# Kernel tuning notes

Measured on AMD Instinct MI355X. Metric: run time of the kernel, lower is better.

The kernel has to match this reference:

```python
import jax, jax.numpy as jnp
import numpy as np

DIM = 512
NUM_HEADS = 8
HEAD_DIM = DIM // NUM_HEADS
FFN_MULT = 4
B, N = 4, 2048
EPS = 1e-5


def setup_inputs() -> dict:
    key = jax.random.key(0)
    ks = jax.random.split(key, 12)
    s = 0.02
    return {
        "H": jax.random.normal(ks[0], (B, N, DIM), jnp.float32),
        "A": jax.random.uniform(ks[1], (B, N, N), jnp.float32),
        "ln1_g": jnp.ones((DIM,), jnp.float32),
        "ln1_b": jnp.zeros((DIM,), jnp.float32),
        "qkv_w": jax.random.normal(ks[2], (DIM, 3 * DIM), jnp.float32) * s,
        "qkv_b": jnp.zeros((3 * DIM,), jnp.float32),
        "proj_w": jax.random.normal(ks[3], (DIM, DIM), jnp.float32) * s,
        "proj_b": jnp.zeros((DIM,), jnp.float32),
        "ln2_g": jnp.ones((DIM,), jnp.float32),
        "ln2_b": jnp.zeros((DIM,), jnp.float32),
        "w1": jax.random.normal(ks[4], (DIM, DIM * FFN_MULT), jnp.float32) * s,
        "b1": jnp.zeros((DIM * FFN_MULT,), jnp.float32),
        "w2": jax.random.normal(ks[5], (DIM * FFN_MULT, DIM), jnp.float32) * s,
        "b2": jnp.zeros((DIM,), jnp.float32),
        "edge_w": jax.random.normal(ks[6], (NUM_HEADS,), jnp.float32) * 0.5,
        "edge_scale": jnp.float32(0.1),
    }


def _layernorm(x, g, b):
    mu = jnp.mean(x, axis=-1, keepdims=True)
    var = jnp.mean(jnp.square(x - mu), axis=-1, keepdims=True)
    return (x - mu) * jax.lax.rsqrt(var + EPS) * g + b


def reference(H, A, ln1_g, ln1_b, qkv_w, qkv_b, proj_w, proj_b,
              ln2_g, ln2_b, w1, b1, w2, b2, edge_w, edge_scale):
    scale = HEAD_DIM ** -0.5
    x = _layernorm(H, ln1_g, ln1_b)
    qkv = (x @ qkv_w + qkv_b).reshape(B, N, 3, NUM_HEADS, HEAD_DIM)
    q = qkv[:, :, 0].transpose(0, 2, 1, 3)  # (B, h, N, d)
    k = qkv[:, :, 1].transpose(0, 2, 1, 3)
    v = qkv[:, :, 2].transpose(0, 2, 1, 3)
    attn = jnp.einsum("bhnd,bhmd->bhnm", q, k) * scale
    # edge bias: Linear(1->H) applied to A[...,None] is A[b,i,j]*edge_w[h]
    bias = edge_scale * edge_w[None, :, None, None] * A[:, None, :, :]
    attn = jax.nn.softmax(attn + bias, axis=-1)
    out = jnp.einsum("bhnm,bhmd->bhnd", attn, v)
    out = out.transpose(0, 2, 1, 3).reshape(B, N, DIM)
    H = H + out @ proj_w + proj_b
    y = _layernorm(H, ln2_g, ln2_b)
    y = jax.nn.gelu(y @ w1 + b1, approximate=False) @ w2 + b2
    return H + y
```

## Files before the change

kernel.cpp:

```cpp
#include <hip/hip_runtime.h>
#include <hip/hip_bf16.h>

#define DIM 512
#define NHEAD 8
#define HD 64
#define SEQ 2048
#define BATCH 4
#define NROWS (BATCH * SEQ)

typedef __bf16 bf16;
typedef __bf16 bf16x8 __attribute__((ext_vector_type(8)));
typedef __bf16 bf16x4 __attribute__((ext_vector_type(4)));
typedef float f32x4 __attribute__((ext_vector_type(4)));
typedef unsigned short us8 __attribute__((ext_vector_type(8)));
typedef unsigned int u32x4 __attribute__((ext_vector_type(4)));

__device__ __forceinline__ f32x4 mfma16(bf16x8 a, bf16x8 b, f32x4 c) {
  return __builtin_amdgcn_mfma_f32_16x16x32_bf16(a, b, c, 0, 0, 0);
}

__device__ __forceinline__ void gload16(const bf16* g, bf16* l) {
  __builtin_amdgcn_global_load_lds((const __attribute__((address_space(1))) void*)g,
                                   (__attribute__((address_space(3))) void*)l, 16, 0, 0);
}

__global__ __launch_bounds__(512, 2) void permute_a(const float* __restrict__ A,
                                                    bf16* __restrict__ out) {
  const int jt = blockIdx.x, it = blockIdx.y, b = blockIdx.z;
  const int t = threadIdx.x;
  const int ql = t & 15, kg = (t >> 4) & 3, wave = t >> 6;
#pragma unroll
  for (int mf = 0; mf < 2; mf++) {
    const int row = it * 256 + wave * 32 + mf * 16 + ql;
    const float* arow = A + ((size_t)b * SEQ + row) * SEQ + jt * 128 + kg * 4;
    bf16* obase = out + ((((size_t)((b * 8 + it) * 16 + jt) * 2 + mf) * 4) * 512 + t) * 8;
#pragma unroll
    for (int c = 0; c < 4; c++) {
      float4 lo = *(const float4*)(arow + (2 * c) * 16);
      float4 hi = *(const float4*)(arow + (2 * c) * 16 + 16);
      bf16x8 o;
      o[0] = (bf16)lo.x; o[1] = (bf16)lo.y; o[2] = (bf16)lo.z; o[3] = (bf16)lo.w;
      o[4] = (bf16)hi.x; o[5] = (bf16)hi.y; o[6] = (bf16)hi.z; o[7] = (bf16)hi.w;
      *(bf16x8*)(obase + (size_t)c * 512 * 8) = o;
    }
  }
}

__global__ __launch_bounds__(256, 8) void convert_all(
    const float* __restrict__ s0, const float* __restrict__ s1, const float* __restrict__ s2,
    const float* __restrict__ s3, bf16* __restrict__ d0, bf16* __restrict__ d1,
    bf16* __restrict__ d2, bf16* __restrict__ d3) {
  __shared__ float tile[32][33];
  int id = blockIdx.x;
  const float* src;
  bf16* dst;
  int R, C, tid;
  if (id < 768) {
    src = s0; dst = d0; R = 512; C = 1536; tid = id;
  } else if (id < 1024) {
    src = s1; dst = d1; R = 512; C = 512; tid = id - 768;
  } else if (id < 2048) {
    src = s2; dst = d2; R = 512; C = 2048; tid = id - 1024;
  } else {
    src = s3; dst = d3; R = 2048; C = 512; tid = id - 2048;
  }
  const int cw = C / 32;
  const int bx = tid % cw, by = tid / cw;
  const int tx = threadIdx.x & 31, ty = threadIdx.x >> 5;
#pragma unroll
  for (int i = 0; i < 32; i += 8)
    tile[ty + i][tx] = src[(size_t)(by * 32 + ty + i) * C + bx * 32 + tx];
  __syncthreads();
#pragma unroll
  for (int i = 0; i < 32; i += 8)
    dst[(size_t)(bx * 32 + ty + i) * R + by * 32 + tx] = (bf16)tile[tx][ty + i];
}

__global__ __launch_bounds__(256, 8) void ln_kernel(const float* __restrict__ in,
                                                    const float* __restrict__ g,
                                                    const float* __restrict__ b,
                                                    bf16* __restrict__ out) {
  int row = blockIdx.x * 4 + (threadIdx.x >> 6);
  int lane = threadIdx.x & 63;
  const float4* p = (const float4*)(in + (size_t)row * DIM);
  float4 v0 = p[lane];
  float4 v1 = p[lane + 64];
  float s = v0.x + v0.y + v0.z + v0.w + v1.x + v1.y + v1.z + v1.w;
#pragma unroll
  for (int m = 1; m < 64; m <<= 1) s += __shfl_xor(s, m);
  float mean = s * (1.0f / DIM);
  float d0 = v0.x - mean, d1 = v0.y - mean, d2 = v0.z - mean, d3 = v0.w - mean;
  float d4 = v1.x - mean, d5 = v1.y - mean, d6 = v1.z - mean, d7 = v1.w - mean;
  float q = d0 * d0 + d1 * d1 + d2 * d2 + d3 * d3 + d4 * d4 + d5 * d5 + d6 * d6 + d7 * d7;
#pragma unroll
  for (int m = 1; m < 64; m <<= 1) q += __shfl_xor(q, m);
  float rstd = rsqrtf(q * (1.0f / DIM) + 1e-5f);
  const float4* gp = (const float4*)g;
  const float4* bp = (const float4*)b;
  float4 g0 = gp[lane], g1 = gp[lane + 64];
  float4 b0 = bp[lane], b1 = bp[lane + 64];
  bf16x4 oa, ob;
  oa[0] = (bf16)(d0 * rstd * g0.x + b0.x);
  oa[1] = (bf16)(d1 * rstd * g0.y + b0.y);
  oa[2] = (bf16)(d2 * rstd * g0.z + b0.z);
  oa[3] = (bf16)(d3 * rstd * g0.w + b0.w);
  ob[0] = (bf16)(d4 * rstd * g1.x + b1.x);
  ob[1] = (bf16)(d5 * rstd * g1.y + b1.y);
  ob[2] = (bf16)(d6 * rstd * g1.z + b1.z);
  ob[3] = (bf16)(d7 * rstd * g1.w + b1.w);
  *(bf16x4*)(out + (size_t)row * DIM + lane * 4) = oa;
  *(bf16x4*)(out + (size_t)row * DIM + 256 + lane * 4) = ob;
}

#define GBM 128
#define GBN 128
#define GBK 64

enum { EPI_BF16 = 0, EPI_GELU = 1, EPI_RESID = 2 };

template <int EPI>
__global__ __launch_bounds__(256, 4) void gemm_bt(const bf16* __restrict__ A,
                                                  const bf16* __restrict__ Bt,
                                                  const float* __restrict__ bias,
                                                  const float* resid, void* outv,
                                                  int M, int N, int K) {
  __shared__ bf16 Al[GBM * GBK];
  __shared__ bf16 Bl[GBN * GBK];
  const int t = threadIdx.x;
  const int lane = t & 63;
  const int wave = t >> 6;
  const int wm = wave >> 1, wn = wave & 1;

  const int gx = gridDim.x;
  const int nwg = gx * gridDim.y;
  const int rawid = blockIdx.y * gx + blockIdx.x;
  const int q = nwg >> 3, r = nwg & 7;
  const int xcd = rawid & 7, pos = rawid >> 3;
  const int wgid = (xcd < r ? xcd * (q + 1) : r * (q + 1) + (xcd - r) * q) + pos;
  const int m0 = (wgid / gx) * GBM, n0 = (wgid % gx) * GBN;

  f32x4 acc[4][4] = {};

  const int srow0 = wave * 32 + (lane >> 3);
  const int scol = (lane & 7) * 8;
  const bf16* ga = A + (size_t)(m0 + srow0) * K + scol;
  const bf16* gb = Bt + (size_t)(n0 + srow0) * K + scol;
  bf16* lA = &Al[wave * 32 * GBK];
  bf16* lB = &Bl[wave * 32 * GBK];

#pragma unroll
  for (int i = 0; i < 4; i++) gload16(ga + (size_t)i * 8 * K, lA + i * 8 * GBK);
#pragma unroll
  for (int i = 0; i < 4; i++) gload16(gb + (size_t)i * 8 * K, lB + i * 8 * GBK);

  for (int k0 = 0; k0 < K; k0 += GBK) {
    __syncthreads();
#pragma unroll
    for (int kk = 0; kk < GBK; kk += 32) {
      bf16x8 af[4], bfr[4];
#pragma unroll
      for (int i = 0; i < 4; i++)
        af[i] = *(const bf16x8*)&Al[(wm * 64 + i * 16 + (lane & 15)) * GBK + kk + (lane >> 4) * 8];
#pragma unroll
      for (int j = 0; j < 4; j++)
        bfr[j] = *(const bf16x8*)&Bl[(wn * 64 + j * 16 + (lane & 15)) * GBK + kk + (lane >> 4) * 8];
#pragma unroll
      for (int i = 0; i < 4; i++)
#pragma unroll
        for (int j = 0; j < 4; j++) acc[i][j] = mfma16(af[i], bfr[j], acc[i][j]);
    }
    __syncthreads();
    if (k0 + GBK < K) {
      ga += GBK;
      gb += GBK;
#pragma unroll
      for (int i = 0; i < 4; i++) gload16(ga + (size_t)i * 8 * K, lA + i * 8 * GBK);
#pragma unroll
      for (int i = 0; i < 4; i++) gload16(gb + (size_t)i * 8 * K, lB + i * 8 * GBK);
    }
  }
  const int rbase = (lane >> 4) * 4;
  const int cl = lane & 15;
#pragma unroll
  for (int i = 0; i < 4; i++) {
#pragma unroll
    for (int j = 0; j < 4; j++) {
      int col = n0 + wn * 64 + j * 16 + cl;
      float bv = bias[col];
#pragma unroll
      for (int r2 = 0; r2 < 4; r2++) {
        int row = m0 + wm * 64 + i * 16 + rbase + r2;
        float v = acc[i][j][r2] + bv;
        size_t idx = (size_t)row * N + col;
        if constexpr (EPI == EPI_BF16) {
          ((bf16*)outv)[idx] = (bf16)v;
        } else if constexpr (EPI == EPI_GELU) {
          ((bf16*)outv)[idx] = (bf16)(0.5f * v * (1.0f + erff(v * 0.70710678118f)));
        } else {
          ((float*)outv)[idx] = resid[idx] + v;
        }
      }
    }
  }
}

__global__ __launch_bounds__(512, 2) void attn_kernel(const bf16* __restrict__ qkv,
                                                      const bf16* __restrict__ Aperm,
                                                      const float* __restrict__ edge_w,
                                                      const float* __restrict__ edge_scale,
                                                      bf16* __restrict__ out) {
  __shared__ bf16 Kl[2][128 * 64];
  __shared__ bf16 Vt[2][64 * 128];
  __shared__ bf16 Pl[8][2][16 * 128];
  const int it = blockIdx.x;
  const int i0 = it * 256;
  const int h = blockIdx.y;
  const int b = blockIdx.z;
  const int t = threadIdx.x, lane = t & 63, wave = t >> 6;
  const int ql = lane & 15;
  const int kg = lane >> 4;
  const int q7 = ql & 7;
  const float LOG2E = 1.44269504089f;
  const float esf = edge_scale[0] * edge_w[h] * LOG2E;

  const int rs = 3 * DIM;
  const bf16* qbase = qkv + (size_t)b * SEQ * rs + h * HD;
  const bf16* kbase = qbase + DIM;
  const bf16* vbase = qbase + 2 * DIM;

  bf16x8 qf[2][2];
#pragma unroll
  for (int mf = 0; mf < 2; mf++)
#pragma unroll
    for (int kf = 0; kf < 2; kf++) {
      bf16x8 q0 = *(const bf16x8*)(qbase + (size_t)(i0 + wave * 32 + mf * 16 + ql) * rs +
                                   kf * 32 + kg * 8);
#pragma unroll
      for (int e = 0; e < 8; e++) q0[e] = (bf16)((float)q0[e] * (0.125f * LOG2E));
      qf[mf][kf] = q0;
    }

  bf16x8 vones;
#pragma unroll
  for (int e = 0; e < 8; e++) vones[e] = (bf16)1.0f;

  const bf16* abase = Aperm + ((size_t)(b * 8 + it) * 16 * 8) * 4096 + (size_t)t * 8;

  float mreg[2] = {-1e30f, -1e30f};
  f32x4 lsum[2] = {};
  f32x4 oacc[2][4] = {};

  const int srow = t >> 2, sq4 = t & 3;
  const int jp = t & 63, doct = t >> 6;

  u32x4 rk0, rk1;
  us8 va0, va1;
  bf16x8 av[2][4];
  {
    const bf16* krow = kbase + (size_t)srow * rs + sq4 * 16;
    rk0 = *(const u32x4*)(krow);
    rk1 = *(const u32x4*)(krow + 8);
    const bf16* vr0 = vbase + (size_t)(2 * jp) * rs + doct * 8;
    va0 = *(const us8*)(vr0);
    va1 = *(const us8*)(vr0 + rs);
  }
  {
    *(u32x4*)&Kl[0][srow * 64 + (((2 * sq4 + 0) ^ (srow & 7)) << 3)] = rk0;
    *(u32x4*)&Kl[0][srow * 64 + (((2 * sq4 + 1) ^ (srow & 7)) << 3)] = rk1;
#pragma unroll
    for (int jj = 0; jj < 8; jj++) {
      unsigned w0 = (unsigned)va0[jj] | ((unsigned)va1[jj] << 16);
      *(unsigned*)&Vt[0][(doct * 8 + jj) * 128 + (((jp >> 2) ^ jj) << 3) + 2 * (jp & 3)] = w0;
    }
  }
  {
    const bf16* krow = kbase + (size_t)(128 + srow) * rs + sq4 * 16;
    rk0 = *(const u32x4*)(krow);
    rk1 = *(const u32x4*)(krow + 8);
    const bf16* vr0 = vbase + (size_t)(128 + 2 * jp) * rs + doct * 8;
    va0 = *(const us8*)(vr0);
    va1 = *(const us8*)(vr0 + rs);
#pragma unroll
    for (int mf = 0; mf < 2; mf++)
#pragma unroll
      for (int c = 0; c < 4; c++)
        av[mf][c] = *(const bf16x8*)(abase + (size_t)(mf * 4 + c) * 4096);
  }
  __syncthreads();

  for (int jtid = 0; jtid < SEQ / 128; jtid++) {
    const int cur = jtid & 1;

    f32x4 st[2][8];
#pragma unroll
    for (int mf = 0; mf < 2; mf++)
#pragma unroll
      for (int c = 0; c < 4; c++)
#pragma unroll
        for (int r = 0; r < 4; r++) {
          st[mf][2 * c][r] = esf * (float)av[mf][c][r];
          st[mf][2 * c + 1][r] = esf * (float)av[mf][c][4 + r];
        }
    if (jtid + 1 < SEQ / 128) {
#pragma unroll
      for (int mf = 0; mf < 2; mf++)
#pragma unroll
        for (int c = 0; c < 4; c++)
          av[mf][c] = *(const bf16x8*)(abase + (size_t)((jtid + 1) * 8 + mf * 4 + c) * 4096);
    }

    __builtin_amdgcn_s_setprio(1);
#pragma unroll
    for (int kf = 0; kf < 2; kf++)
#pragma unroll
      for (int nf = 0; nf < 8; nf++) {
        bf16x8 kfr =
            *(const bf16x8*)&Kl[cur][(nf * 16 + ql) * 64 + ((((kf << 2) + kg) ^ q7) << 3)];
        st[0][nf] = mfma16(kfr, qf[0][kf], st[0][nf]);
        st[1][nf] = mfma16(kfr, qf[1][kf], st[1][nf]);
      }
    __builtin_amdgcn_s_setprio(0);

    if (jtid + 1 < SEQ / 128) {
      *(u32x4*)&Kl[cur ^ 1][srow * 64 + (((2 * sq4 + 0) ^ (srow & 7)) << 3)] = rk0;
      *(u32x4*)&Kl[cur ^ 1][srow * 64 + (((2 * sq4 + 1) ^ (srow & 7)) << 3)] = rk1;
#pragma unroll
      for (int jj = 0; jj < 8; jj++) {
        unsigned w0 = (unsigned)va0[jj] | ((unsigned)va1[jj] << 16);
        *(unsigned*)&Vt[cur ^ 1][(doct * 8 + jj) * 128 + (((jp >> 2) ^ jj) << 3) + 2 * (jp & 3)] =
            w0;
      }
      if (jtid + 2 < SEQ / 128) {
        const int jn = (jtid + 2) * 128;
        const bf16* krow = kbase + (size_t)(jn + srow) * rs + sq4 * 16;
        rk0 = *(const u32x4*)(krow);
        rk1 = *(const u32x4*)(krow + 8);
        const bf16* vr0 = vbase + (size_t)(jn + 2 * jp) * rs + doct * 8;
        va0 = *(const us8*)(vr0);
        va1 = *(const us8*)(vr0 + rs);
      }
    }

#pragma unroll
    for (int mf = 0; mf < 2; mf++) {
      float rmax = st[mf][0][0];
#pragma unroll
      for (int nf = 0; nf < 8; nf++)
#pragma unroll
        for (int r = 0; r < 4; r++) rmax = fmaxf(rmax, st[mf][nf][r]);
      rmax = fmaxf(rmax, __shfl_xor(rmax, 16));
      rmax = fmaxf(rmax, __shfl_xor(rmax, 32));
      if (__any(rmax > mreg[mf] + 8.0f)) {
        float mnew = fmaxf(mreg[mf], rmax);
        float corr = exp2f(mreg[mf] - mnew);
        mreg[mf] = mnew;
#pragma unroll
        for (int r = 0; r < 4; r++) {
          float c = __shfl(corr, kg * 4 + r);
          lsum[mf][r] *= c;
#pragma unroll
          for (int nd = 0; nd < 4; nd++) oacc[mf][nd][r] *= c;
        }
      }
#pragma unroll
      for (int nf = 0; nf < 8; nf++) {
        bf16x4 pk;
#pragma unroll
        for (int r = 0; r < 4; r++) pk[r] = (bf16)exp2f(st[mf][nf][r] - mreg[mf]);
        *(bf16x4*)&Pl[wave][mf][ql * 128 + (((2 * nf + (kg >> 1)) ^ q7) << 3) + (kg & 1) * 4] = pk;
      }
    }

    __builtin_amdgcn_s_setprio(1);
#pragma unroll
    for (int kf = 0; kf < 4; kf++) {
      bf16x8 pa0 = *(const bf16x8*)&Pl[wave][0][ql * 128 + ((((kf << 2) + kg) ^ q7) << 3)];
      bf16x8 pa1 = *(const bf16x8*)&Pl[wave][1][ql * 128 + ((((kf << 2) + kg) ^ q7) << 3)];
      lsum[0] = mfma16(pa0, vones, lsum[0]);
      lsum[1] = mfma16(pa1, vones, lsum[1]);
#pragma unroll
      for (int nd = 0; nd < 4; nd++) {
        bf16x8 vv =
            *(const bf16x8*)&Vt[cur][(nd * 16 + ql) * 128 + ((((kf << 2) + kg) ^ q7) << 3)];
        oacc[0][nd] = mfma16(pa0, vv, oacc[0][nd]);
        oacc[1][nd] = mfma16(pa1, vv, oacc[1][nd]);
      }
    }
    __builtin_amdgcn_s_setprio(0);

    __syncthreads();
  }

#pragma unroll
  for (int mf = 0; mf < 2; mf++)
#pragma unroll
    for (int r = 0; r < 4; r++) {
      float rinv = 1.0f / lsum[mf][r];
      int irow = i0 + wave * 32 + mf * 16 + kg * 4 + r;
      bf16* orow = out + ((size_t)b * SEQ + irow) * DIM + h * HD;
#pragma unroll
      for (int nd = 0; nd < 4; nd++) orow[nd * 16 + ql] = (bf16)(oacc[mf][nd][r] * rinv);
    }
}

constexpr size_t OFF_WQKV = 0;
constexpr size_t OFF_WPROJ = OFF_WQKV + (size_t)1536 * 512 * 2;
constexpr size_t OFF_W1 = OFF_WPROJ + (size_t)512 * 512 * 2;
constexpr size_t OFF_W2 = OFF_W1 + (size_t)2048 * 512 * 2;
constexpr size_t OFF_XW = OFF_W2 + (size_t)512 * 2048 * 2;
constexpr size_t OFF_SHARED = OFF_XW + (size_t)NROWS * DIM * 2;
constexpr size_t OFF_ATTNOUT = OFF_SHARED + (size_t)NROWS * 2048 * 2;
constexpr size_t OFF_APERM = OFF_ATTNOUT + (size_t)NROWS * DIM * 2;
constexpr size_t WS_NEED = OFF_APERM + (size_t)BATCH * SEQ * SEQ * 2;

extern "C" void kernel_launch(void* const* d_in, const int* in_sizes, int n_in,
                              void* d_out, int out_size, void* d_ws, size_t ws_size,
                              hipStream_t stream) {
  const float* H = (const float*)d_in[0];
  const float* A = (const float*)d_in[1];
  const float* ln1_g = (const float*)d_in[2];
  const float* ln1_b = (const float*)d_in[3];
  const float* qkv_w = (const float*)d_in[4];
  const float* qkv_b = (const float*)d_in[5];
  const float* proj_w = (const float*)d_in[6];
  const float* proj_b = (const float*)d_in[7];
  const float* ln2_g = (const float*)d_in[8];
  const float* ln2_b = (const float*)d_in[9];
  const float* w1 = (const float*)d_in[10];
  const float* b1 = (const float*)d_in[11];
  const float* w2 = (const float*)d_in[12];
  const float* b2 = (const float*)d_in[13];
  const float* edge_w = (const float*)d_in[14];
  const float* edge_scale = (const float*)d_in[15];
  float* out = (float*)d_out;
  char* ws = (char*)d_ws;

  bf16* wqkv = (bf16*)(ws + OFF_WQKV);
  bf16* wproj = (bf16*)(ws + OFF_WPROJ);
  bf16* w1t = (bf16*)(ws + OFF_W1);
  bf16* w2t = (bf16*)(ws + OFF_W2);
  bf16* xw = (bf16*)(ws + OFF_XW);
  bf16* qkvb = (bf16*)(ws + OFF_SHARED);
  bf16* ffn1 = (bf16*)(ws + OFF_SHARED);
  bf16* attnout = (bf16*)(ws + OFF_ATTNOUT);
  bf16* aperm = (bf16*)(ws + OFF_APERM);

  permute_a<<<dim3(16, 8, 4), 512, 0, stream>>>(A, aperm);
  convert_all<<<3072, 256, 0, stream>>>(qkv_w, proj_w, w1, w2, wqkv, wproj, w1t, w2t);

  ln_kernel<<<NROWS / 4, 256, 0, stream>>>(H, ln1_g, ln1_b, xw);
  gemm_bt<EPI_BF16><<<dim3(1536 / GBN, NROWS / GBM), 256, 0, stream>>>(
      xw, wqkv, qkv_b, nullptr, qkvb, NROWS, 1536, 512);
  attn_kernel<<<dim3(SEQ / 256, NHEAD, BATCH), 512, 0, stream>>>(qkvb, aperm, edge_w, edge_scale,
                                                                 attnout);
  gemm_bt<EPI_RESID><<<dim3(512 / GBN, NROWS / GBM), 256, 0, stream>>>(
      attnout, wproj, proj_b, H, out, NROWS, 512, 512);
  ln_kernel<<<NROWS / 4, 256, 0, stream>>>(out, ln2_g, ln2_b, xw);
  gemm_bt<EPI_GELU><<<dim3(2048 / GBN, NROWS / GBM), 256, 0, stream>>>(
      xw, w1t, b1, nullptr, ffn1, NROWS, 2048, 512);
  gemm_bt<EPI_RESID><<<dim3(512 / GBN, NROWS / GBM), 256, 0, stream>>>(
      ffn1, w2t, b2, out, out, NROWS, 512, 2048);
}
```

Before: 236.2 us.

## Halve attention block size and pass P through shuffles instead of LDS

Attention blocks now cover 128 query rows with 256 threads instead of 256 rows with 512 threads, so there are twice as many blocks. The permuted A layout, its producer kernel and the K/V staging thread mapping are reworked to match. The per-wave P tile no longer goes through shared memory. Softmax probabilities are packed into registers and redistributed with cross-lane shuffles into the MFMA A-operand layout. This removes the LDS round trip and LDS footprint for P, but adds shuffle instructions and register pressure, and each block's K/V loads are now shared by fewer query rows.

```diff
diff --git a/kernel.cpp b/kernel.cpp
--- a/kernel.cpp
+++ b/kernel.cpp
@@ -14,6 +14,7 @@
 typedef float f32x4 __attribute__((ext_vector_type(4)));
 typedef unsigned short us8 __attribute__((ext_vector_type(8)));
 typedef unsigned int u32x4 __attribute__((ext_vector_type(4)));
+typedef unsigned int u32x2 __attribute__((ext_vector_type(2)));
 
 __device__ __forceinline__ f32x4 mfma16(bf16x8 a, bf16x8 b, f32x4 c) {
   return __builtin_amdgcn_mfma_f32_16x16x32_bf16(a, b, c, 0, 0, 0);
@@ -24,16 +25,16 @@
                                    (__attribute__((address_space(3))) void*)l, 16, 0, 0);
 }
 
-__global__ __launch_bounds__(512, 2) void permute_a(const float* __restrict__ A,
+__global__ __launch_bounds__(256, 4) void permute_a(const float* __restrict__ A,
                                                     bf16* __restrict__ out) {
   const int jt = blockIdx.x, it = blockIdx.y, b = blockIdx.z;
   const int t = threadIdx.x;
   const int ql = t & 15, kg = (t >> 4) & 3, wave = t >> 6;
 #pragma unroll
   for (int mf = 0; mf < 2; mf++) {
-    const int row = it * 256 + wave * 32 + mf * 16 + ql;
+    const int row = it * 128 + wave * 32 + mf * 16 + ql;
     const float* arow = A + ((size_t)b * SEQ + row) * SEQ + jt * 128 + kg * 4;
-    bf16* obase = out + ((((size_t)((b * 8 + it) * 16 + jt) * 2 + mf) * 4) * 512 + t) * 8;
+    bf16* obase = out + ((((size_t)((b * 16 + it) * 16 + jt) * 2 + mf) * 4) * 256 + t) * 8;
 #pragma unroll
     for (int c = 0; c < 4; c++) {
       float4 lo = *(const float4*)(arow + (2 * c) * 16);
@@ -41,7 +42,7 @@
       bf16x8 o;
       o[0] = (bf16)lo.x; o[1] = (bf16)lo.y; o[2] = (bf16)lo.z; o[3] = (bf16)lo.w;
       o[4] = (bf16)hi.x; o[5] = (bf16)hi.y; o[6] = (bf16)hi.z; o[7] = (bf16)hi.w;
-      *(bf16x8*)(obase + (size_t)c * 512 * 8) = o;
+      *(bf16x8*)(obase + (size_t)c * 256 * 8) = o;
     }
   }
 }
@@ -204,22 +205,24 @@
   }
 }
 
-__global__ __launch_bounds__(512, 2) void attn_kernel(const bf16* __restrict__ qkv,
+__global__ __launch_bounds__(256, 2) void attn_kernel(const bf16* __restrict__ qkv,
                                                       const bf16* __restrict__ Aperm,
                                                       const float* __restrict__ edge_w,
                                                       const float* __restrict__ edge_scale,
                                                       bf16* __restrict__ out) {
   __shared__ bf16 Kl[2][128 * 64];
   __shared__ bf16 Vt[2][64 * 128];
-  __shared__ bf16 Pl[8][2][16 * 128];
   const int it = blockIdx.x;
-  const int i0 = it * 256;
+  const int i0 = it * 128;
   const int h = blockIdx.y;
   const int b = blockIdx.z;
   const int t = threadIdx.x, lane = t & 63, wave = t >> 6;
   const int ql = lane & 15;
   const int kg = lane >> 4;
   const int q7 = ql & 7;
+  const int sl0 = ql + ((lane & 16) << 1);
+  const int sl1 = sl0 + 16;
+  const bool up = (lane & 32) != 0;
   const float LOG2E = 1.44269504089f;
   const float esf = edge_scale[0] * edge_w[h] * LOG2E;
 
@@ -244,47 +247,51 @@
 #pragma unroll
   for (int e = 0; e < 8; e++) vones[e] = (bf16)1.0f;
 
-  const bf16* abase = Aperm + ((size_t)(b * 8 + it) * 16 * 8) * 4096 + (size_t)t * 8;
+  const bf16* abase = Aperm + (size_t)(b * 16 + it) * 262144 + (size_t)t * 8;
 
   float mreg[2] = {-1e30f, -1e30f};
   f32x4 lsum[2] = {};
   f32x4 oacc[2][4] = {};
 
-  const int srow = t >> 2, sq4 = t & 3;
-  const int jp = t & 63, doct = t >> 6;
-
-  u32x4 rk0, rk1;
-  us8 va0, va1;
+  const int srow = t >> 1, shalf = t & 1;
+  const int vo = t >> 5, vjq = t & 31;
+
+  u32x4 rk[4];
+  us8 va[4];
   bf16x8 av[2][4];
+
   {
-    const bf16* krow = kbase + (size_t)srow * rs + sq4 * 16;
-    rk0 = *(const u32x4*)(krow);
-    rk1 = *(const u32x4*)(krow + 8);
-    const bf16* vr0 = vbase + (size_t)(2 * jp) * rs + doct * 8;
-    va0 = *(const us8*)(vr0);
-    va1 = *(const us8*)(vr0 + rs);
+    const bf16* krow = kbase + (size_t)srow * rs + shalf * 32;
+#pragma unroll
+    for (int i = 0; i < 4; i++) rk[i] = *(const u32x4*)(krow + i * 8);
+#pragma unroll
+    for (int jj = 0; jj < 4; jj++)
+      va[jj] = *(const us8*)(vbase + (size_t)(4 * vjq + jj) * rs + vo * 8);
   }
   {
-    *(u32x4*)&Kl[0][srow * 64 + (((2 * sq4 + 0) ^ (srow & 7)) << 3)] = rk0;
-    *(u32x4*)&Kl[0][srow * 64 + (((2 * sq4 + 1) ^ (srow & 7)) << 3)] = rk1;
-#pragma unroll
-    for (int jj = 0; jj < 8; jj++) {
-      unsigned w0 = (unsigned)va0[jj] | ((unsigned)va1[jj] << 16);
-      *(unsigned*)&Vt[0][(doct * 8 + jj) * 128 + (((jp >> 2) ^ jj) << 3) + 2 * (jp & 3)] = w0;
+#pragma unroll
+    for (int i = 0; i < 4; i++)
+      *(u32x4*)&Kl[0][srow * 64 + (((shalf * 4 + i) ^ (srow & 7)) << 3)] = rk[i];
+#pragma unroll
+    for (int e = 0; e < 8; e++) {
+      u32x2 w;
+      w[0] = (unsigned)va[0][e] | ((unsigned)va[1][e] << 16);
+      w[1] = (unsigned)va[2][e] | ((unsigned)va[3][e] << 16);
+      *(u32x2*)&Vt[0][(vo * 8 + e) * 128 + (((vjq >> 1) ^ e) << 3) + ((vjq & 1) << 2)] = w;
     }
   }
   {
-    const bf16* krow = kbase + (size_t)(128 + srow) * rs + sq4 * 16;
-    rk0 = *(const u32x4*)(krow);
-    rk1 = *(const u32x4*)(krow + 8);
-    const bf16* vr0 = vbase + (size_t)(128 + 2 * jp) * rs + doct * 8;
-    va0 = *(const us8*)(vr0);
-    va1 = *(const us8*)(vr0 + rs);
+    const bf16* krow = kbase + (size_t)(128 + srow) * rs + shalf * 32;
+#pragma unroll
+    for (int i = 0; i < 4; i++) rk[i] = *(const u32x4*)(krow + i * 8);
+#pragma unroll
+    for (int jj = 0; jj < 4; jj++)
+      va[jj] = *(const us8*)(vbase + (size_t)(128 + 4 * vjq + jj) * rs + vo * 8);
 #pragma unroll
     for (int mf = 0; mf < 2; mf++)
 #pragma unroll
       for (int c = 0; c < 4; c++)
-        av[mf][c] = *(const bf16x8*)(abase + (size_t)(mf * 4 + c) * 4096);
+        av[mf][c] = *(const bf16x8*)(abase + (size_t)(mf * 4 + c) * 2048);
   }
   __syncthreads();
 
@@ -306,7 +313,7 @@
       for (int mf = 0; mf < 2; mf++)
 #pragma unroll
         for (int c = 0; c < 4; c++)
-          av[mf][c] = *(const bf16x8*)(abase + (size_t)((jtid + 1) * 8 + mf * 4 + c) * 4096);
+          av[mf][c] = *(const bf16x8*)(abase + (size_t)((jtid + 1) * 8 + mf * 4 + c) * 2048);
     }
 
     __builtin_amdgcn_s_setprio(1);
@@ -322,25 +329,28 @@
     __builtin_amdgcn_s_setprio(0);
 
     if (jtid + 1 < SEQ / 128) {
-      *(u32x4*)&Kl[cur ^ 1][srow * 64 + (((2 * sq4 + 0) ^ (srow & 7)) << 3)] = rk0;
-      *(u32x4*)&Kl[cur ^ 1][srow * 64 + (((2 * sq4 + 1) ^ (srow & 7)) << 3)] = rk1;
-#pragma unroll
-      for (int jj = 0; jj < 8; jj++) {
-        unsigned w0 = (unsigned)va0[jj] | ((unsigned)va1[jj] << 16);
-        *(unsigned*)&Vt[cur ^ 1][(doct * 8 + jj) * 128 + (((jp >> 2) ^ jj) << 3) + 2 * (jp & 3)] =
-            w0;
+#pragma unroll
+      for (int i = 0; i < 4; i++)
+        *(u32x4*)&Kl[cur ^ 1][srow * 64 + (((shalf * 4 + i) ^ (srow & 7)) << 3)] = rk[i];
+#pragma unroll
+      for (int e = 0; e < 8; e++) {
+        u32x2 w;
+        w[0] = (unsigned)va[0][e] | ((unsigned)va[1][e] << 16);
+        w[1] = (unsigned)va[2][e] | ((unsigned)va[3][e] << 16);
+        *(u32x2*)&Vt[cur ^ 1][(vo * 8 + e) * 128 + (((vjq >> 1) ^ e) << 3) + ((vjq & 1) << 2)] = w;
       }
       if (jtid + 2 < SEQ / 128) {
         const int jn = (jtid + 2) * 128;
-        const bf16* krow = kbase + (size_t)(jn + srow) * rs + sq4 * 16;
-        rk0 = *(const u32x4*)(krow);
-        rk1 = *(const u32x4*)(krow + 8);
-        const bf16* vr0 = vbase + (size_t)(jn + 2 * jp) * rs + doct * 8;
-        va0 = *(const us8*)(vr0);
-        va1 = *(const us8*)(vr0 + rs);
-      }
-    }
-
+        const bf16* krow = kbase + (size_t)(jn + srow) * rs + shalf * 32;
+#pragma unroll
+        for (int i = 0; i < 4; i++) rk[i] = *(const u32x4*)(krow + i * 8);
+#pragma unroll
+        for (int jj = 0; jj < 4; jj++)
+          va[jj] = *(const us8*)(vbase + (size_t)(jn + 4 * vjq + jj) * rs + vo * 8);
+      }
+    }
+
+    unsigned wlo[2][8], whi[2][8];
 #pragma unroll
     for (int mf = 0; mf < 2; mf++) {
       float rmax = st[mf][0][0];
@@ -364,26 +374,49 @@
       }
 #pragma unroll
       for (int nf = 0; nf < 8; nf++) {
-        bf16x4 pk;
-#pragma unroll
-        for (int r = 0; r < 4; r++) pk[r] = (bf16)exp2f(st[mf][nf][r] - mreg[mf]);
-        *(bf16x4*)&Pl[wave][mf][ql * 128 + (((2 * nf + (kg >> 1)) ^ q7) << 3) + (kg & 1) * 4] = pk;
+        union {
+          bf16x4 v;
+          unsigned u[2];
+        } U;
+#pragma unroll
+        for (int r = 0; r < 4; r++) U.v[r] = (bf16)exp2f(st[mf][nf][r] - mreg[mf]);
+        wlo[mf][nf] = U.u[0];
+        whi[mf][nf] = U.u[1];
       }
     }
 
     __builtin_amdgcn_s_setprio(1);
 #pragma unroll
     for (int kf = 0; kf < 4; kf++) {
-      bf16x8 pa0 = *(const bf16x8*)&Pl[wave][0][ql * 128 + ((((kf << 2) + kg) ^ q7) << 3)];
-      bf16x8 pa1 = *(const bf16x8*)&Pl[wave][1][ql * 128 + ((((kf << 2) + kg) ^ q7) << 3)];
-      lsum[0] = mfma16(pa0, vones, lsum[0]);
-      lsum[1] = mfma16(pa1, vones, lsum[1]);
+      bf16x8 pa[2];
+#pragma unroll
+      for (int mf = 0; mf < 2; mf++) {
+        unsigned a0 = (unsigned)__shfl((int)wlo[mf][2 * kf], sl0);
+        unsigned a1 = (unsigned)__shfl((int)whi[mf][2 * kf], sl0);
+        unsigned b0 = (unsigned)__shfl((int)wlo[mf][2 * kf + 1], sl0);
+        unsigned b1 = (unsigned)__shfl((int)whi[mf][2 * kf + 1], sl0);
+        unsigned c0 = (unsigned)__shfl((int)wlo[mf][2 * kf], sl1);
+        unsigned c1 = (unsigned)__shfl((int)whi[mf][2 * kf], sl1);
+        unsigned d0 = (unsigned)__shfl((int)wlo[mf][2 * kf + 1], sl1);
+        unsigned d1 = (unsigned)__shfl((int)whi[mf][2 * kf + 1], sl1);
+        union {
+          unsigned u[4];
+          bf16x8 v;
+        } U;
+        U.u[0] = up ? b0 : a0;
+        U.u[1] = up ? b1 : a1;
+        U.u[2] = up ? d0 : c0;
+        U.u[3] = up ? d1 : c1;
+        pa[mf] = U.v;
+      }
+      lsum[0] = mfma16(pa[0], vones, lsum[0]);
+      lsum[1] = mfma16(pa[1], vones, lsum[1]);
 #pragma unroll
       for (int nd = 0; nd < 4; nd++) {
         bf16x8 vv =
             *(const bf16x8*)&Vt[cur][(nd * 16 + ql) * 128 + ((((kf << 2) + kg) ^ q7) << 3)];
-        oacc[0][nd] = mfma16(pa0, vv, oacc[0][nd]);
-        oacc[1][nd] = mfma16(pa1, vv, oacc[1][nd]);
+        oacc[0][nd] = mfma16(pa[0], vv, oacc[0][nd]);
+        oacc[1][nd] = mfma16(pa[1], vv, oacc[1][nd]);
       }
     }
     __builtin_amdgcn_s_setprio(0);
@@ -445,13 +478,13 @@
   bf16* attnout = (bf16*)(ws + OFF_ATTNOUT);
   bf16* aperm = (bf16*)(ws + OFF_APERM);
 
-  permute_a<<<dim3(16, 8, 4), 512, 0, stream>>>(A, aperm);
+  permute_a<<<dim3(16, 16, 4), 256, 0, stream>>>(A, aperm);
   convert_all<<<3072, 256, 0, stream>>>(qkv_w, proj_w, w1, w2, wqkv, wproj, w1t, w2t);
 
   ln_kernel<<<NROWS / 4, 256, 0, stream>>>(H, ln1_g, ln1_b, xw);
   gemm_bt<EPI_BF16><<<dim3(1536 / GBN, NROWS / GBM), 256, 0, stream>>>(
       xw, wqkv, qkv_b, nullptr, qkvb, NROWS, 1536, 512);
-  attn_kernel<<<dim3(SEQ / 256, NHEAD, BATCH), 512, 0, stream>>>(qkvb, aperm, edge_w, edge_scale,
+  attn_kernel<<<dim3(SEQ / 128, NHEAD, BATCH), 256, 0, stream>>>(qkvb, aperm, edge_w, edge_scale,
                                                                  attnout);
   gemm_bt<EPI_RESID><<<dim3(512 / GBN, NROWS / GBM), 256, 0, stream>>>(
       attnout, wproj, proj_b, H, out, NROWS, 512, 512);
```

Measured after the change: 260.0 us. +10.1%, slower.
